# Kernel optimization log

Measured on AMD Instinct MI355X. Metric: run time of the kernel, lower is better.

## Reference

```python
import jax, jax.numpy as jnp
import numpy as np

B, T, I, H = 64, 512, 512, 512

def setup_inputs() -> dict:
    key = jax.random.key(0)
    ks = jax.random.split(key, 13)
    s = 0.02
    return {
        'inputs': jax.random.normal(ks[0], (B, T, I), dtype=jnp.float32),
        'W_i': jax.random.normal(ks[1], (I, H), dtype=jnp.float32) * s,
        'W_f': jax.random.normal(ks[2], (I, H), dtype=jnp.float32) * s,
        'W_o': jax.random.normal(ks[3], (I, H), dtype=jnp.float32) * s,
        'W_c': jax.random.normal(ks[4], (I, H), dtype=jnp.float32) * s,
        'U_i': jax.random.normal(ks[5], (H, H), dtype=jnp.float32) * s,
        'U_f': jax.random.normal(ks[6], (H, H), dtype=jnp.float32) * s,
        'U_o': jax.random.normal(ks[7], (H, H), dtype=jnp.float32) * s,
        'U_c': jax.random.normal(ks[8], (H, H), dtype=jnp.float32) * s,
        'b_i': jax.random.normal(ks[9], (1, H), dtype=jnp.float32) * s,
        'b_f': jax.random.normal(ks[10], (1, H), dtype=jnp.float32) * s,
        'b_o': jax.random.normal(ks[11], (1, H), dtype=jnp.float32) * s,
        'b_c': jax.random.normal(ks[12], (1, H), dtype=jnp.float32) * s,
    }

def reference(inputs, W_i, W_f, W_o, W_c, U_i, U_f, U_o, U_c, b_i, b_f, b_o, b_c):
    batch = inputs.shape[0]
    hidden = U_i.shape[0]
    # Precompute input projections for all 4 gates in one fused GEMM: [T, B, 4H]
    W = jnp.concatenate([W_i, W_f, W_o, W_c], axis=1)          # [I, 4H]
    b = jnp.concatenate([b_i, b_f, b_o, b_c], axis=1)          # [1, 4H]
    U = jnp.concatenate([U_i, U_f, U_o, U_c], axis=1)          # [H, 4H]
    x_proj = jnp.einsum('bti,ig->tbg', inputs, W) + b          # [T, B, 4H]

    def step(carry, xg):
        h, c = carry
        g = xg + h @ U                                          # [B, 4H]
        i_g = jax.nn.sigmoid(g[:, 0*hidden:1*hidden])
        f_g = jax.nn.sigmoid(g[:, 1*hidden:2*hidden])
        o_g = jax.nn.sigmoid(g[:, 2*hidden:3*hidden])
        c_t = jnp.tanh(g[:, 3*hidden:4*hidden])
        c = f_g * c + i_g * c_t
        h = o_g * jnp.tanh(c)
        return (h, c), None

    h0 = jnp.zeros((batch, hidden), dtype=inputs.dtype)
    c0 = jnp.zeros((batch, hidden), dtype=inputs.dtype)
    (h, c), _ = jax.lax.scan(step, (h0, c0), x_proj)
    return h
```

## Files before the change

kernel.cpp:

```cpp
#include <hip/hip_runtime.h>
#include <hip/hip_bf16.h>
#include <cstdint>


typedef __bf16 bf16;
typedef __bf16 bf16x8 __attribute__((ext_vector_type(8)));
typedef float floatx4 __attribute__((ext_vector_type(4)));
typedef uint64_t u64;
typedef uint32_t u32;

#define T_STEPS 512

#define XP_OFF     0ull
#define XBF_OFF    134217728ull
#define WCT_OFF    167772160ull
#define USW_OFF    169869312ull
#define BCAT_OFF   171966464ull
#define HBUF_OFF   171974656ull

__device__ inline u32 pack_bf16x2(float a, float b) {
    union { __bf16 h[2]; u32 u; } cv;
    cv.h[0] = (__bf16)a; cv.h[1] = (__bf16)b;
    return cv.u;
}
__device__ inline float bf_lo(u32 w) { return __builtin_bit_cast(float, w << 16); }
__device__ inline float bf_hi(u32 w) { return __builtin_bit_cast(float, w & 0xffff0000u); }

__device__ inline void lgkm_barrier() {
    __atomic_signal_fence(__ATOMIC_SEQ_CST);
    __builtin_amdgcn_s_waitcnt(0xc07f);
    __builtin_amdgcn_s_barrier();
    __atomic_signal_fence(__ATOMIC_SEQ_CST);
}

__device__ inline void wave_lds_fence() {
    __atomic_signal_fence(__ATOMIC_SEQ_CST);
    __builtin_amdgcn_s_waitcnt(0xc07f);
    __builtin_amdgcn_sched_barrier(0);
    __atomic_signal_fence(__ATOMIC_SEQ_CST);
}

__global__ void k0a_convert(const float* __restrict__ in, bf16* __restrict__ xbf) {
    int o = blockIdx.x * 256 + threadIdx.x;
    int k = o & 511;
    int r = o >> 9;
    int t = r >> 6, b = r & 63;
    xbf[o] = (bf16)in[(b * 512 + t) * 512 + k];
}

__global__ void k0b_wcat(const float* __restrict__ Wi, const float* __restrict__ Wf,
                         const float* __restrict__ Wo, const float* __restrict__ Wc,
                         const float* __restrict__ bi, const float* __restrict__ bfv,
                         const float* __restrict__ bo, const float* __restrict__ bc,
                         bf16* __restrict__ wct, float* __restrict__ bcat) {
    int o = blockIdx.x * 256 + threadIdx.x;
    int k = o & 511;
    int c = o >> 9;
    int h = c >> 2, g = c & 3;
    const float* W = (g == 0) ? Wi : (g == 1) ? Wf : (g == 2) ? Wo : Wc;
    wct[o] = (bf16)W[k * 512 + h];
    if (o < 2048) {
        int hh = o >> 2, gg = o & 3;
        const float* bv = (gg == 0) ? bi : (gg == 1) ? bfv : (gg == 2) ? bo : bc;
        bcat[o] = bv[hh];
    }
}

__global__ void k0c_uswz(const float* __restrict__ Ui, const float* __restrict__ Uf,
                         const float* __restrict__ Uo, const float* __restrict__ Uc,
                         bf16* __restrict__ usw) {
    int o = blockIdx.x * 256 + threadIdx.x;
    int e  = o & 7;
    int l  = (o >> 3) & 63;
    int ks = (o >> 9) & 15;
    int nt = (o >> 13) & 1;
    int w  = (o >> 14) & 3;
    int s  = o >> 16;
    int k = ks * 32 + (l >> 4) * 8 + e;
    int col_local = (2 * w + nt) * 16 + (l & 15);
    int h = s * 32 + (col_local >> 2);
    int g = col_local & 3;
    const float* U = (g == 0) ? Ui : (g == 1) ? Uf : (g == 2) ? Uo : Uc;
    usw[o] = (bf16)U[k * 512 + h];
}

__launch_bounds__(256, 2)
__global__ void k1_gemm(const bf16* __restrict__ xbf, const bf16* __restrict__ wct,
                        const float* __restrict__ bcat, bf16* __restrict__ xp) {
    __shared__ bf16 As[128 * 40];
    __shared__ bf16 Bs[128 * 40];
    int tid = threadIdx.x;
    int wid = tid >> 6, lane = tid & 63;
    int q = lane >> 4, m = lane & 15;
    int wr = wid >> 1, wc = wid & 1;
    int br = blockIdx.x & 255, bc = blockIdx.x >> 8;

    floatx4 acc[4][4] = {};

    for (int kk = 0; kk < 16; ++kk) {
        #pragma unroll
        for (int cc = 0; cc < 2; ++cc) {
            int ch = tid + cc * 256;
            int row = ch >> 2, part = ch & 3;
            bf16x8 va = *(const bf16x8*)&xbf[(br * 128 + row) * 512 + kk * 32 + part * 8];
            bf16x8 vb = *(const bf16x8*)&wct[(bc * 128 + row) * 512 + kk * 32 + part * 8];
            *(bf16x8*)&As[row * 40 + part * 8] = va;
            *(bf16x8*)&Bs[row * 40 + part * 8] = vb;
        }
        __syncthreads();
        bf16x8 af[4], bfr[4];
        #pragma unroll
        for (int i = 0; i < 4; ++i) {
            af[i]  = *(const bf16x8*)&As[(wr * 64 + i * 16 + m) * 40 + q * 8];
            bfr[i] = *(const bf16x8*)&Bs[(wc * 64 + i * 16 + m) * 40 + q * 8];
        }
        #pragma unroll
        for (int mt = 0; mt < 4; ++mt)
            #pragma unroll
            for (int nt = 0; nt < 4; ++nt)
                acc[mt][nt] = __builtin_amdgcn_mfma_f32_16x16x32_bf16(
                    af[mt], bfr[nt], acc[mt][nt], 0, 0, 0);
        __syncthreads();
    }
    float bias[4];
    #pragma unroll
    for (int nt = 0; nt < 4; ++nt) bias[nt] = bcat[bc * 128 + wc * 64 + nt * 16 + m];
    #pragma unroll
    for (int mt = 0; mt < 4; ++mt) {
        #pragma unroll
        for (int nt = 0; nt < 4; ++nt) {
            u32 p0 = pack_bf16x2(acc[mt][nt][0] + bias[nt], acc[mt][nt][1] + bias[nt]);
            u32 p1 = pack_bf16x2(acc[mt][nt][2] + bias[nt], acc[mt][nt][3] + bias[nt]);
            size_t idx = (((((size_t)(br * 2 + wr) * 4 + mt) * 16 + bc) * 8
                           + wc * 4 + nt) * 64 + lane) * 4;
            uint2 v; v.x = p0; v.y = p1;
            *(uint2*)&xp[idx] = v;
        }
    }
}

__launch_bounds__(256, 1)
__global__ void k2_rec(const bf16* __restrict__ xp, const bf16* __restrict__ usw,
                       u64* __restrict__ hbuf, float* __restrict__ out) {
    __shared__ u32 h_sh[2][16 * 256];
    __shared__ float g_slab[4][16 * 36];

    int tid = threadIdx.x;
    int wid = tid >> 6, lane = tid & 63;
    int q = lane >> 4, m = lane & 15;
    int bg = blockIdx.x & 3, s = blockIdx.x >> 2;

    bf16x8 bfr[2][16];
    {
        const bf16x8* base = (const bf16x8*)usw;
        #pragma unroll
        for (int nt = 0; nt < 2; ++nt)
            #pragma unroll
            for (int ks = 0; ks < 16; ++ks)
                bfr[nt][ks] = base[(((s * 4 + wid) * 2 + nt) * 16 + ks) * 64 + lane];
    }

    int r2 = lane >> 2;
    int kk2 = lane & 3;
    float cs0 = 0.f, cs1 = 0.f;

    int wc = tid >> 2, wk = tid & 3;

    float* gs = &g_slab[wid][0];

    uint2 vx0, vx1;
    {
        size_t b0 = ((((size_t)bg * 16 + s) * 8 + wid * 2) * 64 + lane) * 4;
        vx0 = *(const uint2*)&xp[b0];
        vx1 = *(const uint2*)&xp[b0 + 256];
    }

    for (int t = 0; t < T_STEPS; ++t) {
        floatx4 acc[2];

        acc[0][0] = bf_lo(vx0.x); acc[0][1] = bf_hi(vx0.x);
        acc[0][2] = bf_lo(vx0.y); acc[0][3] = bf_hi(vx0.y);
        acc[1][0] = bf_lo(vx1.x); acc[1][1] = bf_hi(vx1.x);
        acc[1][2] = bf_lo(vx1.y); acc[1][3] = bf_hi(vx1.y);

        if (t > 0) {
            __atomic_signal_fence(__ATOMIC_SEQ_CST);
            __builtin_amdgcn_s_sleep(8);
            __atomic_signal_fence(__ATOMIC_SEQ_CST);

            const u64* rb = hbuf + ((size_t)((t - 1) & 1) * 4 + bg) * 4096;
            u32 tg = (u32)t;
            u64 w[16];
            #pragma unroll
            for (int i = 0; i < 16; ++i)
                w[i] = __hip_atomic_load(rb + tid + 256 * i, __ATOMIC_RELAXED,
                                         __HIP_MEMORY_SCOPE_AGENT);
            for (;;) {
                bool ok = true;
                #pragma unroll
                for (int i = 0; i < 16; ++i) ok &= ((u32)(w[i] >> 32) == tg);
                if (ok) break;
                #pragma unroll
                for (int i = 0; i < 16; ++i)
                    w[i] = __hip_atomic_load(rb + tid + 256 * i, __ATOMIC_RELAXED,
                                             __HIP_MEMORY_SCOPE_AGENT);
            }
            u32* hp = &h_sh[(t & 1) ^ 1][0];
            #pragma unroll
            for (int i = 0; i < 16; ++i)
                hp[i * 256 + ((wc ^ (i & 7)) << 2) + wk] = (u32)w[i];
            lgkm_barrier();
            const bf16* hbs = (const bf16*)hp;
            #pragma unroll
            for (int ks = 0; ks < 16; ++ks) {
                bf16x8 af = *(const bf16x8*)&hbs[m * 512 + (((4 * ks + q) ^ (m & 7)) << 3)];
                acc[0] = __builtin_amdgcn_mfma_f32_16x16x32_bf16(af, bfr[0][ks], acc[0], 0, 0, 0);
                acc[1] = __builtin_amdgcn_mfma_f32_16x16x32_bf16(af, bfr[1][ks], acc[1], 0, 0, 0);
            }
        }

        if (t + 1 < T_STEPS) {
            size_t b0 = (((((size_t)(t + 1) * 4 + bg) * 16 + s) * 8 + wid * 2) * 64 + lane) * 4;
            vx0 = *(const uint2*)&xp[b0];
            vx1 = *(const uint2*)&xp[b0 + 256];
        }

        #pragma unroll
        for (int nt = 0; nt < 2; ++nt)
            #pragma unroll
            for (int rr = 0; rr < 4; ++rr)
                gs[(q * 4 + rr) * 36 + nt * 16 + m] = acc[nt][rr];
        wave_lds_fence();

        floatx4 ga = *(const floatx4*)&gs[r2 * 36 + kk2 * 8];
        floatx4 gb = *(const floatx4*)&gs[r2 * 36 + kk2 * 8 + 4];
        float h0, h1;
        {
            float ig = 1.f / (1.f + __expf(-ga[0]));
            float fg = 1.f / (1.f + __expf(-ga[1]));
            float og = 1.f / (1.f + __expf(-ga[2]));
            float th = 1.f - 2.f / (__expf(2.f * ga[3]) + 1.f);
            cs0 = fg * cs0 + ig * th;
            h0 = og * (1.f - 2.f / (__expf(2.f * cs0) + 1.f));
        }
        {
            float ig = 1.f / (1.f + __expf(-gb[0]));
            float fg = 1.f / (1.f + __expf(-gb[1]));
            float og = 1.f / (1.f + __expf(-gb[2]));
            float th = 1.f - 2.f / (__expf(2.f * gb[3]) + 1.f);
            cs1 = fg * cs1 + ig * th;
            h1 = og * (1.f - 2.f / (__expf(2.f * cs1) + 1.f));
        }
        u64 word = ((u64)(u32)(t + 1) << 32) | (u64)pack_bf16x2(h0, h1);
        __hip_atomic_store(hbuf + (((size_t)(t & 1) * 4 + bg) * 16 + r2) * 256
                                + s * 16 + wid * 4 + kk2,
                           word, __ATOMIC_RELAXED, __HIP_MEMORY_SCOPE_AGENT);
        if (t == T_STEPS - 1) {
            int u0 = s * 32 + wid * 8 + kk2 * 2;
            out[(bg * 16 + r2) * 512 + u0]     = h0;
            out[(bg * 16 + r2) * 512 + u0 + 1] = h1;
        }
    }
}

extern "C" void kernel_launch(void* const* d_in, const int* in_sizes, int n_in,
                              void* d_out, int out_size, void* d_ws, size_t ws_size,
                              hipStream_t stream) {
    const float* inp = (const float*)d_in[0];
    const float* Wi  = (const float*)d_in[1];
    const float* Wf  = (const float*)d_in[2];
    const float* Wo  = (const float*)d_in[3];
    const float* Wc  = (const float*)d_in[4];
    const float* Ui  = (const float*)d_in[5];
    const float* Uf  = (const float*)d_in[6];
    const float* Uo  = (const float*)d_in[7];
    const float* Uc  = (const float*)d_in[8];
    const float* bi  = (const float*)d_in[9];
    const float* bfv = (const float*)d_in[10];
    const float* bo  = (const float*)d_in[11];
    const float* bc  = (const float*)d_in[12];

    char* ws = (char*)d_ws;
    bf16*  xp    = (bf16*)(ws + XP_OFF);
    bf16*  xbf   = (bf16*)(ws + XBF_OFF);
    bf16*  wct   = (bf16*)(ws + WCT_OFF);
    bf16*  usw   = (bf16*)(ws + USW_OFF);
    float* bcat  = (float*)(ws + BCAT_OFF);
    u64*   hbuf  = (u64*)(ws + HBUF_OFF);

    k0a_convert<<<65536, 256, 0, stream>>>(inp, xbf);
    k0b_wcat<<<4096, 256, 0, stream>>>(Wi, Wf, Wo, Wc, bi, bfv, bo, bc, wct, bcat);
    k0c_uswz<<<4096, 256, 0, stream>>>(Ui, Uf, Uo, Uc, usw);
    k1_gemm<<<4096, 256, 0, stream>>>(xbf, wct, bcat, xp);
    k2_rec<<<64, 256, 0, stream>>>(xp, usw, hbuf, (float*)d_out);
}
```

Before: 1.426 ms.

## Process two batch groups per recurrent block to interleave sync with compute

The recurrent kernel now runs on 32 blocks, each handling two batch groups in turn within every timestep, so one group's MFMA and gate math can overlap the other group's wait for peer hidden-state publication. It also drops the fixed s_sleep before polling, re-polls only the words that are not yet ready, and splits the MFMA k-loop into two independent accumulator chains for more instruction-level parallelism. The cost is half as many CUs on the serial critical path, so each block does twice the work per step and uses twice the LDS.

```diff
diff --git a/kernel.cpp b/kernel.cpp
--- a/kernel.cpp
+++ b/kernel.cpp
@@ -142,13 +142,15 @@
 __launch_bounds__(256, 1)
 __global__ void k2_rec(const bf16* __restrict__ xp, const bf16* __restrict__ usw,
                        u64* __restrict__ hbuf, float* __restrict__ out) {
-    __shared__ u32 h_sh[2][16 * 256];
+    __shared__ u32 h_sh[2][2][16 * 256];
     __shared__ float g_slab[4][16 * 36];
 
     int tid = threadIdx.x;
     int wid = tid >> 6, lane = tid & 63;
     int q = lane >> 4, m = lane & 15;
-    int bg = blockIdx.x & 3, s = blockIdx.x >> 2;
+    int bid = blockIdx.x;
+    int s   = bid >> 1;
+    int bgA = (bid & 1) * 2;
 
     bf16x8 bfr[2][16];
     {
@@ -162,103 +164,114 @@
 
     int r2 = lane >> 2;
     int kk2 = lane & 3;
-    float cs0 = 0.f, cs1 = 0.f;
+    float cs0[2] = {0.f, 0.f}, cs1[2] = {0.f, 0.f};
 
     int wc = tid >> 2, wk = tid & 3;
 
     float* gs = &g_slab[wid][0];
 
-    uint2 vx0, vx1;
-    {
-        size_t b0 = ((((size_t)bg * 16 + s) * 8 + wid * 2) * 64 + lane) * 4;
-        vx0 = *(const uint2*)&xp[b0];
-        vx1 = *(const uint2*)&xp[b0 + 256];
+    uint2 vxa[2], vxb[2];
+    #pragma unroll
+    for (int p = 0; p < 2; ++p) {
+        size_t b0 = ((((size_t)(bgA + p) * 16 + s) * 8 + wid * 2) * 64 + lane) * 4;
+        vxa[p] = *(const uint2*)&xp[b0];
+        vxb[p] = *(const uint2*)&xp[b0 + 256];
     }
 
     for (int t = 0; t < T_STEPS; ++t) {
-        floatx4 acc[2];
-
-        acc[0][0] = bf_lo(vx0.x); acc[0][1] = bf_hi(vx0.x);
-        acc[0][2] = bf_lo(vx0.y); acc[0][3] = bf_hi(vx0.y);
-        acc[1][0] = bf_lo(vx1.x); acc[1][1] = bf_hi(vx1.x);
-        acc[1][2] = bf_lo(vx1.y); acc[1][3] = bf_hi(vx1.y);
-
-        if (t > 0) {
-            __atomic_signal_fence(__ATOMIC_SEQ_CST);
-            __builtin_amdgcn_s_sleep(8);
-            __atomic_signal_fence(__ATOMIC_SEQ_CST);
-
-            const u64* rb = hbuf + ((size_t)((t - 1) & 1) * 4 + bg) * 4096;
-            u32 tg = (u32)t;
-            u64 w[16];
-            #pragma unroll
-            for (int i = 0; i < 16; ++i)
-                w[i] = __hip_atomic_load(rb + tid + 256 * i, __ATOMIC_RELAXED,
-                                         __HIP_MEMORY_SCOPE_AGENT);
-            for (;;) {
-                bool ok = true;
-                #pragma unroll
-                for (int i = 0; i < 16; ++i) ok &= ((u32)(w[i] >> 32) == tg);
-                if (ok) break;
+        #pragma unroll
+        for (int p = 0; p < 2; ++p) {
+            int bg = bgA + p;
+            floatx4 acc[2];
+
+            acc[0][0] = bf_lo(vxa[p].x); acc[0][1] = bf_hi(vxa[p].x);
+            acc[0][2] = bf_lo(vxa[p].y); acc[0][3] = bf_hi(vxa[p].y);
+            acc[1][0] = bf_lo(vxb[p].x); acc[1][1] = bf_hi(vxb[p].x);
+            acc[1][2] = bf_lo(vxb[p].y); acc[1][3] = bf_hi(vxb[p].y);
+
+            if (t > 0) {
+                const u64* rb = hbuf + ((size_t)((t - 1) & 1) * 4 + bg) * 4096;
+                u32 tg = (u32)t;
+                u64 w[16];
                 #pragma unroll
                 for (int i = 0; i < 16; ++i)
                     w[i] = __hip_atomic_load(rb + tid + 256 * i, __ATOMIC_RELAXED,
                                              __HIP_MEMORY_SCOPE_AGENT);
-            }
-            u32* hp = &h_sh[(t & 1) ^ 1][0];
+                for (;;) {
+                    bool ok = true;
+                    #pragma unroll
+                    for (int i = 0; i < 16; ++i) ok &= ((u32)(w[i] >> 32) == tg);
+                    if (ok) break;
+                    #pragma unroll
+                    for (int i = 0; i < 16; ++i)
+                        if ((u32)(w[i] >> 32) != tg)
+                            w[i] = __hip_atomic_load(rb + tid + 256 * i, __ATOMIC_RELAXED,
+                                                     __HIP_MEMORY_SCOPE_AGENT);
+                }
+                u32* hp = &h_sh[p][(t & 1) ^ 1][0];
+                #pragma unroll
+                for (int i = 0; i < 16; ++i)
+                    hp[i * 256 + ((wc ^ (i & 7)) << 2) + wk] = (u32)w[i];
+                lgkm_barrier();
+                const bf16* hbs = (const bf16*)hp;
+                floatx4 accb0 = {}, accb1 = {};
+                #pragma unroll
+                for (int ks = 0; ks < 8; ++ks) {
+                    bf16x8 af = *(const bf16x8*)&hbs[m * 512 + (((4 * ks + q) ^ (m & 7)) << 3)];
+                    acc[0] = __builtin_amdgcn_mfma_f32_16x16x32_bf16(af, bfr[0][ks], acc[0], 0, 0, 0);
+                    acc[1] = __builtin_amdgcn_mfma_f32_16x16x32_bf16(af, bfr[1][ks], acc[1], 0, 0, 0);
+                }
+                #pragma unroll
+                for (int ks = 8; ks < 16; ++ks) {
+                    bf16x8 af = *(const bf16x8*)&hbs[m * 512 + (((4 * ks + q) ^ (m & 7)) << 3)];
+                    accb0 = __builtin_amdgcn_mfma_f32_16x16x32_bf16(af, bfr[0][ks], accb0, 0, 0, 0);
+                    accb1 = __builtin_amdgcn_mfma_f32_16x16x32_bf16(af, bfr[1][ks], accb1, 0, 0, 0);
+                }
+                acc[0] += accb0;
+                acc[1] += accb1;
+            }
+
+            if (t + 1 < T_STEPS) {
+                size_t b0 = (((((size_t)(t + 1) * 4 + bg) * 16 + s) * 8 + wid * 2) * 64 + lane) * 4;
+                vxa[p] = *(const uint2*)&xp[b0];
+                vxb[p] = *(const uint2*)&xp[b0 + 256];
+            }
+
             #pragma unroll
-            for (int i = 0; i < 16; ++i)
-                hp[i * 256 + ((wc ^ (i & 7)) << 2) + wk] = (u32)w[i];
-            lgkm_barrier();
-            const bf16* hbs = (const bf16*)hp;
-            #pragma unroll
-            for (int ks = 0; ks < 16; ++ks) {
-                bf16x8 af = *(const bf16x8*)&hbs[m * 512 + (((4 * ks + q) ^ (m & 7)) << 3)];
-                acc[0] = __builtin_amdgcn_mfma_f32_16x16x32_bf16(af, bfr[0][ks], acc[0], 0, 0, 0);
-                acc[1] = __builtin_amdgcn_mfma_f32_16x16x32_bf16(af, bfr[1][ks], acc[1], 0, 0, 0);
-            }
-        }
-
-        if (t + 1 < T_STEPS) {
-            size_t b0 = (((((size_t)(t + 1) * 4 + bg) * 16 + s) * 8 + wid * 2) * 64 + lane) * 4;
-            vx0 = *(const uint2*)&xp[b0];
-            vx1 = *(const uint2*)&xp[b0 + 256];
-        }
-
-        #pragma unroll
-        for (int nt = 0; nt < 2; ++nt)
-            #pragma unroll
-            for (int rr = 0; rr < 4; ++rr)
-                gs[(q * 4 + rr) * 36 + nt * 16 + m] = acc[nt][rr];
-        wave_lds_fence();
-
-        floatx4 ga = *(const floatx4*)&gs[r2 * 36 + kk2 * 8];
-        floatx4 gb = *(const floatx4*)&gs[r2 * 36 + kk2 * 8 + 4];
-        float h0, h1;
-        {
-            float ig = 1.f / (1.f + __expf(-ga[0]));
-            float fg = 1.f / (1.f + __expf(-ga[1]));
-            float og = 1.f / (1.f + __expf(-ga[2]));
-            float th = 1.f - 2.f / (__expf(2.f * ga[3]) + 1.f);
-            cs0 = fg * cs0 + ig * th;
-            h0 = og * (1.f - 2.f / (__expf(2.f * cs0) + 1.f));
-        }
-        {
-            float ig = 1.f / (1.f + __expf(-gb[0]));
-            float fg = 1.f / (1.f + __expf(-gb[1]));
-            float og = 1.f / (1.f + __expf(-gb[2]));
-            float th = 1.f - 2.f / (__expf(2.f * gb[3]) + 1.f);
-            cs1 = fg * cs1 + ig * th;
-            h1 = og * (1.f - 2.f / (__expf(2.f * cs1) + 1.f));
-        }
-        u64 word = ((u64)(u32)(t + 1) << 32) | (u64)pack_bf16x2(h0, h1);
-        __hip_atomic_store(hbuf + (((size_t)(t & 1) * 4 + bg) * 16 + r2) * 256
-                                + s * 16 + wid * 4 + kk2,
-                           word, __ATOMIC_RELAXED, __HIP_MEMORY_SCOPE_AGENT);
-        if (t == T_STEPS - 1) {
-            int u0 = s * 32 + wid * 8 + kk2 * 2;
-            out[(bg * 16 + r2) * 512 + u0]     = h0;
-            out[(bg * 16 + r2) * 512 + u0 + 1] = h1;
+            for (int nt = 0; nt < 2; ++nt)
+                #pragma unroll
+                for (int rr = 0; rr < 4; ++rr)
+                    gs[(q * 4 + rr) * 36 + nt * 16 + m] = acc[nt][rr];
+            wave_lds_fence();
+
+            floatx4 ga = *(const floatx4*)&gs[r2 * 36 + kk2 * 8];
+            floatx4 gb = *(const floatx4*)&gs[r2 * 36 + kk2 * 8 + 4];
+            float h0, h1;
+            {
+                float ig = 1.f / (1.f + __expf(-ga[0]));
+                float fg = 1.f / (1.f + __expf(-ga[1]));
+                float og = 1.f / (1.f + __expf(-ga[2]));
+                float th = 1.f - 2.f / (__expf(2.f * ga[3]) + 1.f);
+                cs0[p] = fg * cs0[p] + ig * th;
+                h0 = og * (1.f - 2.f / (__expf(2.f * cs0[p]) + 1.f));
+            }
+            {
+                float ig = 1.f / (1.f + __expf(-gb[0]));
+                float fg = 1.f / (1.f + __expf(-gb[1]));
+                float og = 1.f / (1.f + __expf(-gb[2]));
+                float th = 1.f - 2.f / (__expf(2.f * gb[3]) + 1.f);
+                cs1[p] = fg * cs1[p] + ig * th;
+                h1 = og * (1.f - 2.f / (__expf(2.f * cs1[p]) + 1.f));
+            }
+            u64 word = ((u64)(u32)(t + 1) << 32) | (u64)pack_bf16x2(h0, h1);
+            __hip_atomic_store(hbuf + (((size_t)(t & 1) * 4 + bg) * 16 + r2) * 256
+                                    + s * 16 + wid * 4 + kk2,
+                               word, __ATOMIC_RELAXED, __HIP_MEMORY_SCOPE_AGENT);
+            if (t == T_STEPS - 1) {
+                int u0 = s * 32 + wid * 8 + kk2 * 2;
+                out[(bg * 16 + r2) * 512 + u0]     = h0;
+                out[(bg * 16 + r2) * 512 + u0 + 1] = h1;
+            }
         }
     }
 }
@@ -292,5 +305,5 @@
     k0b_wcat<<<4096, 256, 0, stream>>>(Wi, Wf, Wo, Wc, bi, bfv, bo, bc, wct, bcat);
     k0c_uswz<<<4096, 256, 0, stream>>>(Ui, Uf, Uo, Uc, usw);
     k1_gemm<<<4096, 256, 0, stream>>>(xbf, wct, bcat, xp);
-    k2_rec<<<64, 256, 0, stream>>>(xp, usw, hbuf, (float*)d_out);
-}
+    k2_rec<<<32, 256, 0, stream>>>(xp, usw, hbuf, (float*)d_out);
+}
```

Result: slower. 2.436 ms (+70.8%).
